# Optimization experiments

Measured on AMD Instinct MI355X. Metric: run time of the kernel, lower is better.

## Reference

```python
import jax, jax.numpy as jnp
import numpy as np

B, T, D, H = 2, 2048, 1024, 16
HD = D // H


def setup_inputs() -> dict:
    key = jax.random.key(0)
    ks = jax.random.split(key, 8)
    s = 1.0 / np.sqrt(D)
    x = jax.random.normal(ks[0], (B, T, D), dtype=jnp.float32)
    # causal additive mask, as in Whisper: -inf-like on strict upper triangle
    mask = jnp.triu(jnp.full((T, T), -1e9, dtype=jnp.float32), k=1)
    Wq = jax.random.normal(ks[1], (D, D), dtype=jnp.float32) * s
    bq = jax.random.normal(ks[2], (D,), dtype=jnp.float32) * 0.02
    Wk = jax.random.normal(ks[3], (D, D), dtype=jnp.float32) * s  # key has no bias
    Wv = jax.random.normal(ks[4], (D, D), dtype=jnp.float32) * s
    bv = jax.random.normal(ks[5], (D,), dtype=jnp.float32) * 0.02
    Wo = jax.random.normal(ks[6], (D, D), dtype=jnp.float32) * s
    bo = jax.random.normal(ks[7], (D,), dtype=jnp.float32) * 0.02
    return {"x": x, "mask": mask, "Wq": Wq, "bq": bq, "Wk": Wk,
            "Wv": Wv, "bv": bv, "Wo": Wo, "bo": bo}


def reference(x, mask, Wq, bq, Wk, Wv, bv, Wo, bo):
    # Linear layers (torch F.linear: x @ W.T + b)
    q = x @ Wq.T + bq                      # [B, T, D]
    k = x @ Wk.T                           # [B, T, D] (no bias)
    v = x @ Wv.T + bv                      # [B, T, D]

    scale = (D // H) ** (-0.25)
    qh = q.reshape(B, T, H, HD) * scale    # [B, T, H, hd]
    kh = k.reshape(B, T, H, HD) * scale
    vh = v.reshape(B, T, H, HD)

    qk = jnp.einsum("bqhd,bkhd->bhqk", qh, kh)        # [B, H, T, T]
    qk = qk + mask[:T, :T]
    w = jax.nn.softmax(qk.astype(jnp.float32), axis=-1).astype(q.dtype)
    wv = jnp.einsum("bhqk,bkhd->bqhd", w, vh).reshape(B, T, D)
    return wv @ Wo.T + bo
```

## Files before the change

kernel.cpp:

```cpp
#include <hip/hip_runtime.h>
#include <hip/hip_bf16.h>

#define B_ 2
#define T_ 2048
#define D_ 1024
#define H_ 16
#define HD_ 64

typedef __attribute__((ext_vector_type(8))) short bf16x8;
typedef __attribute__((ext_vector_type(4))) short bf16x4;
typedef __attribute__((ext_vector_type(4))) float f32x4;
typedef __attribute__((ext_vector_type(4))) unsigned int u32x4;

__device__ __forceinline__ short f2bf(float f) {
  unsigned int u = __builtin_bit_cast(unsigned int, f);
  u += 0x7fffu + ((u >> 16) & 1u);
  return (short)(u >> 16);
}

__device__ __forceinline__ unsigned cvtpk(float lo, float hi) {
  unsigned r;
  asm("v_cvt_pk_bf16_f32 %0, %1, %2" : "=v"(r) : "v"(lo), "v"(hi));
  return r;
}

__device__ __forceinline__ float ex2(float x) {
  float r;
  asm("v_exp_f32 %0, %1" : "=v"(r) : "v"(x));
  return r;
}

__device__ __forceinline__ void gl16(const short* g, short* l) {
  __builtin_amdgcn_global_load_lds(
      (const __attribute__((address_space(1))) void*)g,
      (__attribute__((address_space(3))) void*)l, 16, 0, 0);
}

__global__ void cast_f32_bf16(const float* __restrict__ in, short* __restrict__ out, int n) {
  int i = (blockIdx.x * blockDim.x + threadIdx.x) * 8;
  if (i + 7 >= n) return;
  float4 a = *(const float4*)(in + i);
  float4 b = *(const float4*)(in + i + 4);
  bf16x8 o;
  o[0] = f2bf(a.x); o[1] = f2bf(a.y); o[2] = f2bf(a.z); o[3] = f2bf(a.w);
  o[4] = f2bf(b.x); o[5] = f2bf(b.y); o[6] = f2bf(b.z); o[7] = f2bf(b.w);
  *(bf16x8*)(out + i) = o;
}

__global__ void cast_w4(const float* __restrict__ w0, const float* __restrict__ w1,
                        const float* __restrict__ w2, const float* __restrict__ w3,
                        short* __restrict__ out) {
  int i = (blockIdx.x * blockDim.x + threadIdx.x) * 8;
  int seg = i >> 20;
  const float* src = (seg == 0) ? w0 : (seg == 1) ? w1 : (seg == 2) ? w2 : w3;
  int off = i & 1048575;
  float4 a = *(const float4*)(src + off);
  float4 b = *(const float4*)(src + off + 4);
  bf16x8 o;
  o[0] = f2bf(a.x); o[1] = f2bf(a.y); o[2] = f2bf(a.z); o[3] = f2bf(a.w);
  o[4] = f2bf(b.x); o[5] = f2bf(b.y); o[6] = f2bf(b.z); o[7] = f2bf(b.w);
  *(bf16x8*)(out + i) = o;
}

__launch_bounds__(256, 3)
__global__ void gemm_qkv(const short* __restrict__ A, const short* __restrict__ W,
                         const float* __restrict__ bq, const float* __restrict__ bv,
                         short* __restrict__ Qb, short* __restrict__ Kb,
                         short* __restrict__ Vtb) {
  __shared__ short As[2][64 * 64];
  __shared__ short Bs[2][128 * 64];
  const int bm = blockIdx.x / 24, bn = blockIdx.x % 24;
  const int tid = threadIdx.x, lane = tid & 63, w = tid >> 6;
  const int wr = w >> 1, wc = w & 1;
  const int lrow = lane & 15, lhi = lane >> 4;
  const int srow = lane >> 3, sch = lane & 7;
  const int swz = (lrow & 7) << 3;

  f32x4 acc[2][4] = {};
  auto STAGE = [&](int kt, int buf) {
#pragma unroll
    for (int i = 0; i < 2; ++i) {
      int row = w * 16 + i * 8 + srow;
      gl16(A + (size_t)(bm * 64 + row) * 1024 + kt + ((sch ^ (row & 7)) * 8),
           &As[buf][(w * 16 + i * 8) * 64]);
    }
#pragma unroll
    for (int i = 0; i < 4; ++i) {
      int row = w * 32 + i * 8 + srow;
      gl16(W + (size_t)(bn * 128 + row) * 1024 + kt + ((sch ^ (row & 7)) * 8),
           &Bs[buf][(w * 32 + i * 8) * 64]);
    }
  };

  STAGE(0, 0);
  for (int t = 0; t < 16; ++t) {
    const int buf = t & 1;
    if (t < 15) {
      STAGE((t + 1) * 64, buf ^ 1);
      asm volatile("s_waitcnt vmcnt(6)" ::: "memory");
    } else {
      asm volatile("s_waitcnt vmcnt(0)" ::: "memory");
    }
    __builtin_amdgcn_s_barrier();
    bf16x8 af[2][2], bfr[2][4];
#pragma unroll
    for (int ks = 0; ks < 2; ++ks) {
#pragma unroll
      for (int i = 0; i < 2; ++i)
        af[ks][i] = *(const bf16x8*)(&As[buf][(wr * 32 + i * 16 + lrow) * 64 + ((ks * 32 + lhi * 8) ^ swz)]);
#pragma unroll
      for (int j = 0; j < 4; ++j)
        bfr[ks][j] = *(const bf16x8*)(&Bs[buf][(wc * 64 + j * 16 + lrow) * 64 + ((ks * 32 + lhi * 8) ^ swz)]);
    }
#pragma unroll
    for (int ks = 0; ks < 2; ++ks)
#pragma unroll
      for (int i = 0; i < 2; ++i)
#pragma unroll
        for (int j = 0; j < 4; ++j)
          acc[i][j] = __builtin_amdgcn_mfma_f32_16x16x32_bf16(af[ks][i], bfr[ks][j],
                                                              acc[i][j], 0, 0, 0);
    asm volatile("s_waitcnt lgkmcnt(0)" ::: "memory");
    __builtin_amdgcn_s_barrier();
  }

#pragma unroll
  for (int i = 0; i < 2; ++i)
#pragma unroll
    for (int j = 0; j < 4; ++j) {
      const int m0 = bm * 64 + wr * 32 + i * 16 + lhi * 4;
      const int n = bn * 128 + wc * 64 + j * 16 + lrow;
      const int seg = n >> 10, nloc = n & 1023;
      const int h = nloc >> 6, hd = nloc & 63;
      const int b = m0 >> 11, t0 = m0 & 2047;
      if (seg == 0) {
        float bb = bq[nloc];
#pragma unroll
        for (int r = 0; r < 4; ++r)
          Qb[((size_t)(b * H_ + h) * T_ + t0 + r) * HD_ + hd] =
              f2bf((acc[i][j][r] + bb) * 0.180336880f);
      } else if (seg == 1) {
#pragma unroll
        for (int r = 0; r < 4; ++r)
          Kb[((size_t)(b * H_ + h) * T_ + t0 + r) * HD_ + hd] = f2bf(acc[i][j][r]);
      } else {
        float bb = bv[nloc];
        bf16x4 ov;
#pragma unroll
        for (int r = 0; r < 4; ++r) ov[r] = f2bf(acc[i][j][r] + bb);
        *(bf16x4*)(Vtb + ((size_t)(b * H_ + h) * HD_ + hd) * T_ + t0) = ov;
      }
    }
}

__launch_bounds__(256, 3)
__global__ void gemm_o(const short* __restrict__ A, const short* __restrict__ W,
                       const float* __restrict__ bias, float* __restrict__ out) {
  __shared__ short As[2][64 * 64];
  __shared__ short Bs[2][128 * 64];
  const int bm = blockIdx.x >> 3, bn = blockIdx.x & 7;
  const int tid = threadIdx.x, lane = tid & 63, w = tid >> 6;
  const int wr = w >> 1, wc = w & 1;
  const int lrow = lane & 15, lhi = lane >> 4;
  const int srow = lane >> 3, sch = lane & 7;
  const int swz = (lrow & 7) << 3;

  f32x4 acc[2][4] = {};
  auto STAGE = [&](int kt, int buf) {
#pragma unroll
    for (int i = 0; i < 2; ++i) {
      int row = w * 16 + i * 8 + srow;
      gl16(A + (size_t)(bm * 64 + row) * 1024 + kt + ((sch ^ (row & 7)) * 8),
           &As[buf][(w * 16 + i * 8) * 64]);
    }
#pragma unroll
    for (int i = 0; i < 4; ++i) {
      int row = w * 32 + i * 8 + srow;
      gl16(W + (size_t)(bn * 128 + row) * 1024 + kt + ((sch ^ (row & 7)) * 8),
           &Bs[buf][(w * 32 + i * 8) * 64]);
    }
  };

  STAGE(0, 0);
  for (int t = 0; t < 16; ++t) {
    const int buf = t & 1;
    if (t < 15) {
      STAGE((t + 1) * 64, buf ^ 1);
      asm volatile("s_waitcnt vmcnt(6)" ::: "memory");
    } else {
      asm volatile("s_waitcnt vmcnt(0)" ::: "memory");
    }
    __builtin_amdgcn_s_barrier();
    bf16x8 af[2][2], bfr[2][4];
#pragma unroll
    for (int ks = 0; ks < 2; ++ks) {
#pragma unroll
      for (int i = 0; i < 2; ++i)
        af[ks][i] = *(const bf16x8*)(&As[buf][(wr * 32 + i * 16 + lrow) * 64 + ((ks * 32 + lhi * 8) ^ swz)]);
#pragma unroll
      for (int j = 0; j < 4; ++j)
        bfr[ks][j] = *(const bf16x8*)(&Bs[buf][(wc * 64 + j * 16 + lrow) * 64 + ((ks * 32 + lhi * 8) ^ swz)]);
    }
#pragma unroll
    for (int ks = 0; ks < 2; ++ks)
#pragma unroll
      for (int i = 0; i < 2; ++i)
#pragma unroll
        for (int j = 0; j < 4; ++j)
          acc[i][j] = __builtin_amdgcn_mfma_f32_16x16x32_bf16(af[ks][i], bfr[ks][j],
                                                              acc[i][j], 0, 0, 0);
    asm volatile("s_waitcnt lgkmcnt(0)" ::: "memory");
    __builtin_amdgcn_s_barrier();
  }

#pragma unroll
  for (int i = 0; i < 2; ++i)
#pragma unroll
    for (int j = 0; j < 4; ++j) {
      const int m0 = bm * 64 + wr * 32 + i * 16 + lhi * 4;
      const int n = bn * 128 + wc * 64 + j * 16 + lrow;
      const float bb = bias[n];
#pragma unroll
      for (int r = 0; r < 4; ++r)
        out[(size_t)(m0 + r) * 1024 + n] = acc[i][j][r] + bb;
    }
}

__launch_bounds__(256, 4)
__global__ void attn_kernel(const short* __restrict__ Q, const short* __restrict__ K,
                            const short* __restrict__ Vt, short* __restrict__ Ob) {
  __shared__ short Ks_[2][64 * 64];
  __shared__ short Vs_[2][64 * 64];
  const int tid = threadIdx.x, lane = tid & 63, w = tid >> 6;
  const int lrow = lane & 15, lhi = lane >> 4;
  const int bid = blockIdx.x;
  const int bh = (bid & 7) * 4 + ((bid >> 3) & 3);
  const int x = bid >> 5, g = x & 7, q = x >> 3;
  const int tile = ((q & 1) ? (7 - g) : g) * 4 + q;
  const int b = bh >> 4, h = bh & 15;
  const short* Kbh = K + (size_t)bh * T_ * HD_;
  const short* Vbh = Vt + (size_t)bh * HD_ * T_;

  bf16x8 qf[2];
#pragma unroll
  for (int ks = 0; ks < 2; ++ks)
    qf[ks] = *(const bf16x8*)(Q + ((size_t)bh * T_ + tile * 64 + w * 16 + lrow) * HD_ + ks * 32 + lhi * 8);

  f32x4 oacc[4] = {};
  float lrun = 0.f;
  const int qlocal = w * 16 + lrow;
  const int srow8 = lane >> 3, sch = lane & 7;
  const int swz = (lrow & 7) << 3;

  auto STAGE = [&](int kb, int buf) {
#pragma unroll
    for (int pass = 0; pass < 2; ++pass) {
      int row = pass * 32 + w * 8 + srow8;
      int csrc = (sch ^ (row & 7)) * 8;
      gl16(Kbh + (size_t)(kb * 64 + row) * HD_ + csrc, &Ks_[buf][(pass * 32 + w * 8) * 64]);
      gl16(Vbh + (size_t)row * T_ + kb * 64 + csrc, &Vs_[buf][(pass * 32 + w * 8) * 64]);
    }
  };

  STAGE(0, 0);
  int cur = 0;
  for (int kb = 0; kb <= tile; ++kb) {
    asm volatile("s_waitcnt vmcnt(0) lgkmcnt(0)" ::: "memory");
    __builtin_amdgcn_s_barrier();
    asm volatile("" ::: "memory");
    const short* Kc = Ks_[cur];
    const short* Vc = Vs_[cur];
    bf16x8 kf[4][2];
#pragma unroll
    for (int n = 0; n < 4; ++n)
#pragma unroll
      for (int ks = 0; ks < 2; ++ks)
        kf[n][ks] = *(const bf16x8*)(Kc + (n * 16 + lrow) * 64 + ((ks * 32 + lhi * 8) ^ swz));
    if (kb < tile) STAGE(kb + 1, cur ^ 1);

    f32x4 s[4] = {};
    __builtin_amdgcn_s_setprio(1);
#pragma unroll
    for (int n = 0; n < 4; ++n)
#pragma unroll
      for (int ks = 0; ks < 2; ++ks)
        s[n] = __builtin_amdgcn_mfma_f32_16x16x32_bf16(kf[n][ks], qf[ks], s[n], 0, 0, 0);
    __builtin_amdgcn_s_setprio(0);

    if (kb == tile) {
#pragma unroll
      for (int n = 0; n < 4; ++n)
#pragma unroll
        for (int r = 0; r < 4; ++r)
          if (n * 16 + lhi * 4 + r > qlocal) s[n][r] = -1e9f;
    }

    float p[4][4];
    float ls = 0.f;
#pragma unroll
    for (int n = 0; n < 4; ++n)
#pragma unroll
      for (int r = 0; r < 4; ++r) {
        float e = ex2(s[n][r] - 12.0f);
        p[n][r] = e;
        ls += e;
      }
    lrun += ls;

    u32x4 pw0, pw1;
    pw0[0] = cvtpk(p[0][0], p[0][1]); pw0[1] = cvtpk(p[0][2], p[0][3]);
    pw0[2] = cvtpk(p[1][0], p[1][1]); pw0[3] = cvtpk(p[1][2], p[1][3]);
    pw1[0] = cvtpk(p[2][0], p[2][1]); pw1[1] = cvtpk(p[2][2], p[2][3]);
    pw1[2] = cvtpk(p[3][0], p[3][1]); pw1[3] = cvtpk(p[3][2], p[3][3]);
    bf16x8 pf0 = __builtin_bit_cast(bf16x8, pw0);
    bf16x8 pf1 = __builtin_bit_cast(bf16x8, pw1);

    bf16x8 vf[4][2];
#pragma unroll
    for (int j = 0; j < 4; ++j)
#pragma unroll
      for (int ks = 0; ks < 2; ++ks) {
        bf16x4 lo = *(const bf16x4*)(Vc + (j * 16 + lrow) * 64 + ((ks * 32 + lhi * 4) ^ swz));
        bf16x4 hi = *(const bf16x4*)(Vc + (j * 16 + lrow) * 64 + ((ks * 32 + 16 + lhi * 4) ^ swz));
        bf16x8 v;
        v[0] = lo[0]; v[1] = lo[1]; v[2] = lo[2]; v[3] = lo[3];
        v[4] = hi[0]; v[5] = hi[1]; v[6] = hi[2]; v[7] = hi[3];
        vf[j][ks] = v;
      }
    __builtin_amdgcn_s_setprio(1);
#pragma unroll
    for (int j = 0; j < 4; ++j) {
      oacc[j] = __builtin_amdgcn_mfma_f32_16x16x32_bf16(vf[j][0], pf0, oacc[j], 0, 0, 0);
      oacc[j] = __builtin_amdgcn_mfma_f32_16x16x32_bf16(vf[j][1], pf1, oacc[j], 0, 0, 0);
    }
    __builtin_amdgcn_s_setprio(0);
    cur ^= 1;
  }

  lrun += __shfl_xor(lrun, 16);
  lrun += __shfl_xor(lrun, 32);
  float inv = 1.0f / lrun;
  const int t = tile * 64 + qlocal;
#pragma unroll
  for (int j = 0; j < 4; ++j) {
    bf16x4 ok;
#pragma unroll
    for (int r = 0; r < 4; ++r) ok[r] = f2bf(oacc[j][r] * inv);
    *(bf16x4*)(Ob + (size_t)(b * T_ + t) * D_ + h * 64 + j * 16 + lhi * 4) = ok;
  }
}

extern "C" void kernel_launch(void* const* d_in, const int* in_sizes, int n_in,
                              void* d_out, int out_size, void* d_ws, size_t ws_size,
                              hipStream_t stream) {
  const float* x  = (const float*)d_in[0];
  const float* Wq = (const float*)d_in[2];
  const float* bq = (const float*)d_in[3];
  const float* Wk = (const float*)d_in[4];
  const float* Wv = (const float*)d_in[5];
  const float* bv = (const float*)d_in[6];
  const float* Wo = (const float*)d_in[7];
  const float* bo = (const float*)d_in[8];
  float* out = (float*)d_out;

  const int MT = B_ * T_;
  short* xb  = (short*)d_ws;
  short* wqb = xb  + (size_t)MT * D_;
  short* wkb = wqb + (size_t)D_ * D_;
  short* wvb = wkb + (size_t)D_ * D_;
  short* wob = wvb + (size_t)D_ * D_;
  short* Qb  = wob + (size_t)D_ * D_;
  short* Kb  = Qb  + (size_t)MT * D_;
  short* Vtb = Kb  + (size_t)MT * D_;
  short* Ab  = Vtb + (size_t)MT * D_;

  cast_f32_bf16<<<(MT * D_) / (256 * 8), 256, 0, stream>>>(x, xb, MT * D_);
  cast_w4<<<(4 * D_ * D_) / (256 * 8), 256, 0, stream>>>(Wq, Wk, Wv, Wo, wqb);

  gemm_qkv<<<(MT / 64) * 24, 256, 0, stream>>>(xb, wqb, bq, bv, Qb, Kb, Vtb);

  attn_kernel<<<B_ * H_ * 32, 256, 0, stream>>>(Qb, Kb, Vtb, Ab);

  gemm_o<<<(MT / 64) * 8, 256, 0, stream>>>(Ab, wob, bo, out);
}
```

Baseline: 101.5 us.

## Enlarge GEMM tiles to 128x128, drop double buffering, merge cast kernels

Both projection GEMMs now use 128x128 output tiles with a 4x4 MFMA accumulator per wave instead of 64x128. Each tile loads its operands into a single LDS buffer guarded by __syncthreads, replacing the double-buffered async prefetch. The two f32-to-bf16 cast kernels are merged into one launch covering x and all four weight matrices. Larger tiles raise operand reuse and cut global traffic, but the launch grid halves (256 blocks for gemm_o, 768 for qkv), and removing the prefetch exposes load latency.

```diff
diff --git a/kernel.cpp b/kernel.cpp
--- a/kernel.cpp
+++ b/kernel.cpp
@@ -36,24 +36,20 @@
       (__attribute__((address_space(3))) void*)l, 16, 0, 0);
 }
 
-__global__ void cast_f32_bf16(const float* __restrict__ in, short* __restrict__ out, int n) {
+__global__ void cast_all(const float* __restrict__ x,
+                         const float* __restrict__ w0, const float* __restrict__ w1,
+                         const float* __restrict__ w2, const float* __restrict__ w3,
+                         short* __restrict__ out) {
   int i = (blockIdx.x * blockDim.x + threadIdx.x) * 8;
-  if (i + 7 >= n) return;
-  float4 a = *(const float4*)(in + i);
-  float4 b = *(const float4*)(in + i + 4);
-  bf16x8 o;
-  o[0] = f2bf(a.x); o[1] = f2bf(a.y); o[2] = f2bf(a.z); o[3] = f2bf(a.w);
-  o[4] = f2bf(b.x); o[5] = f2bf(b.y); o[6] = f2bf(b.z); o[7] = f2bf(b.w);
-  *(bf16x8*)(out + i) = o;
-}
-
-__global__ void cast_w4(const float* __restrict__ w0, const float* __restrict__ w1,
-                        const float* __restrict__ w2, const float* __restrict__ w3,
-                        short* __restrict__ out) {
-  int i = (blockIdx.x * blockDim.x + threadIdx.x) * 8;
-  int seg = i >> 20;
-  const float* src = (seg == 0) ? w0 : (seg == 1) ? w1 : (seg == 2) ? w2 : w3;
-  int off = i & 1048575;
+  const float* src;
+  int off;
+  if (i < 4194304) { src = x; off = i; }
+  else {
+    int j = i - 4194304;
+    int seg = j >> 20;
+    src = (seg == 0) ? w0 : (seg == 1) ? w1 : (seg == 2) ? w2 : w3;
+    off = j & 1048575;
+  }
   float4 a = *(const float4*)(src + off);
   float4 b = *(const float4*)(src + off + 4);
   bf16x8 o;
@@ -62,13 +58,13 @@
   *(bf16x8*)(out + i) = o;
 }
 
-__launch_bounds__(256, 3)
+__launch_bounds__(256)
 __global__ void gemm_qkv(const short* __restrict__ A, const short* __restrict__ W,
                          const float* __restrict__ bq, const float* __restrict__ bv,
                          short* __restrict__ Qb, short* __restrict__ Kb,
                          short* __restrict__ Vtb) {
-  __shared__ short As[2][64 * 64];
-  __shared__ short Bs[2][128 * 64];
+  __shared__ short As[128 * 64];
+  __shared__ short Bs[128 * 64];
   const int bm = blockIdx.x / 24, bn = blockIdx.x % 24;
   const int tid = threadIdx.x, lane = tid & 63, w = tid >> 6;
   const int wr = w >> 1, wc = w & 1;
@@ -76,59 +72,43 @@
   const int srow = lane >> 3, sch = lane & 7;
   const int swz = (lrow & 7) << 3;
 
-  f32x4 acc[2][4] = {};
-  auto STAGE = [&](int kt, int buf) {
-#pragma unroll
-    for (int i = 0; i < 2; ++i) {
-      int row = w * 16 + i * 8 + srow;
-      gl16(A + (size_t)(bm * 64 + row) * 1024 + kt + ((sch ^ (row & 7)) * 8),
-           &As[buf][(w * 16 + i * 8) * 64]);
-    }
+  f32x4 acc[4][4] = {};
+
+  for (int t = 0; t < 16; ++t) {
+    const int kt = t * 64;
 #pragma unroll
     for (int i = 0; i < 4; ++i) {
       int row = w * 32 + i * 8 + srow;
+      gl16(A + (size_t)(bm * 128 + row) * 1024 + kt + ((sch ^ (row & 7)) * 8),
+           &As[(w * 32 + i * 8) * 64]);
       gl16(W + (size_t)(bn * 128 + row) * 1024 + kt + ((sch ^ (row & 7)) * 8),
-           &Bs[buf][(w * 32 + i * 8) * 64]);
-    }
-  };
-
-  STAGE(0, 0);
-  for (int t = 0; t < 16; ++t) {
-    const int buf = t & 1;
-    if (t < 15) {
-      STAGE((t + 1) * 64, buf ^ 1);
-      asm volatile("s_waitcnt vmcnt(6)" ::: "memory");
-    } else {
-      asm volatile("s_waitcnt vmcnt(0)" ::: "memory");
-    }
-    __builtin_amdgcn_s_barrier();
-    bf16x8 af[2][2], bfr[2][4];
-#pragma unroll
-    for (int ks = 0; ks < 2; ++ks) {
-#pragma unroll
-      for (int i = 0; i < 2; ++i)
-        af[ks][i] = *(const bf16x8*)(&As[buf][(wr * 32 + i * 16 + lrow) * 64 + ((ks * 32 + lhi * 8) ^ swz)]);
-#pragma unroll
-      for (int j = 0; j < 4; ++j)
-        bfr[ks][j] = *(const bf16x8*)(&Bs[buf][(wc * 64 + j * 16 + lrow) * 64 + ((ks * 32 + lhi * 8) ^ swz)]);
-    }
+           &Bs[(w * 32 + i * 8) * 64]);
+    }
+    __syncthreads();
+    bf16x8 af[2][4], bfr[2][4];
 #pragma unroll
     for (int ks = 0; ks < 2; ++ks)
 #pragma unroll
-      for (int i = 0; i < 2; ++i)
+      for (int i = 0; i < 4; ++i) {
+        af[ks][i]  = *(const bf16x8*)(&As[(wr * 64 + i * 16 + lrow) * 64 + ((ks * 32 + lhi * 8) ^ swz)]);
+        bfr[ks][i] = *(const bf16x8*)(&Bs[(wc * 64 + i * 16 + lrow) * 64 + ((ks * 32 + lhi * 8) ^ swz)]);
+      }
+#pragma unroll
+    for (int ks = 0; ks < 2; ++ks)
+#pragma unroll
+      for (int i = 0; i < 4; ++i)
 #pragma unroll
         for (int j = 0; j < 4; ++j)
           acc[i][j] = __builtin_amdgcn_mfma_f32_16x16x32_bf16(af[ks][i], bfr[ks][j],
                                                               acc[i][j], 0, 0, 0);
-    asm volatile("s_waitcnt lgkmcnt(0)" ::: "memory");
-    __builtin_amdgcn_s_barrier();
-  }
-
-#pragma unroll
-  for (int i = 0; i < 2; ++i)
+    __syncthreads();
+  }
+
+#pragma unroll
+  for (int i = 0; i < 4; ++i)
 #pragma unroll
     for (int j = 0; j < 4; ++j) {
-      const int m0 = bm * 64 + wr * 32 + i * 16 + lhi * 4;
+      const int m0 = bm * 128 + wr * 64 + i * 16 + lhi * 4;
       const int n = bn * 128 + wc * 64 + j * 16 + lrow;
       const int seg = n >> 10, nloc = n & 1023;
       const int h = nloc >> 6, hd = nloc & 63;
@@ -153,11 +133,11 @@
     }
 }
 
-__launch_bounds__(256, 3)
+__launch_bounds__(256)
 __global__ void gemm_o(const short* __restrict__ A, const short* __restrict__ W,
                        const float* __restrict__ bias, float* __restrict__ out) {
-  __shared__ short As[2][64 * 64];
-  __shared__ short Bs[2][128 * 64];
+  __shared__ short As[128 * 64];
+  __shared__ short Bs[128 * 64];
   const int bm = blockIdx.x >> 3, bn = blockIdx.x & 7;
   const int tid = threadIdx.x, lane = tid & 63, w = tid >> 6;
   const int wr = w >> 1, wc = w & 1;
@@ -165,59 +145,43 @@
   const int srow = lane >> 3, sch = lane & 7;
   const int swz = (lrow & 7) << 3;
 
-  f32x4 acc[2][4] = {};
-  auto STAGE = [&](int kt, int buf) {
-#pragma unroll
-    for (int i = 0; i < 2; ++i) {
-      int row = w * 16 + i * 8 + srow;
-      gl16(A + (size_t)(bm * 64 + row) * 1024 + kt + ((sch ^ (row & 7)) * 8),
-           &As[buf][(w * 16 + i * 8) * 64]);
-    }
+  f32x4 acc[4][4] = {};
+
+  for (int t = 0; t < 16; ++t) {
+    const int kt = t * 64;
 #pragma unroll
     for (int i = 0; i < 4; ++i) {
       int row = w * 32 + i * 8 + srow;
+      gl16(A + (size_t)(bm * 128 + row) * 1024 + kt + ((sch ^ (row & 7)) * 8),
+           &As[(w * 32 + i * 8) * 64]);
       gl16(W + (size_t)(bn * 128 + row) * 1024 + kt + ((sch ^ (row & 7)) * 8),
-           &Bs[buf][(w * 32 + i * 8) * 64]);
-    }
-  };
-
-  STAGE(0, 0);
-  for (int t = 0; t < 16; ++t) {
-    const int buf = t & 1;
-    if (t < 15) {
-      STAGE((t + 1) * 64, buf ^ 1);
-      asm volatile("s_waitcnt vmcnt(6)" ::: "memory");
-    } else {
-      asm volatile("s_waitcnt vmcnt(0)" ::: "memory");
-    }
-    __builtin_amdgcn_s_barrier();
-    bf16x8 af[2][2], bfr[2][4];
-#pragma unroll
-    for (int ks = 0; ks < 2; ++ks) {
-#pragma unroll
-      for (int i = 0; i < 2; ++i)
-        af[ks][i] = *(const bf16x8*)(&As[buf][(wr * 32 + i * 16 + lrow) * 64 + ((ks * 32 + lhi * 8) ^ swz)]);
-#pragma unroll
-      for (int j = 0; j < 4; ++j)
-        bfr[ks][j] = *(const bf16x8*)(&Bs[buf][(wc * 64 + j * 16 + lrow) * 64 + ((ks * 32 + lhi * 8) ^ swz)]);
-    }
+           &Bs[(w * 32 + i * 8) * 64]);
+    }
+    __syncthreads();
+    bf16x8 af[2][4], bfr[2][4];
 #pragma unroll
     for (int ks = 0; ks < 2; ++ks)
 #pragma unroll
-      for (int i = 0; i < 2; ++i)
+      for (int i = 0; i < 4; ++i) {
+        af[ks][i]  = *(const bf16x8*)(&As[(wr * 64 + i * 16 + lrow) * 64 + ((ks * 32 + lhi * 8) ^ swz)]);
+        bfr[ks][i] = *(const bf16x8*)(&Bs[(wc * 64 + i * 16 + lrow) * 64 + ((ks * 32 + lhi * 8) ^ swz)]);
+      }
+#pragma unroll
+    for (int ks = 0; ks < 2; ++ks)
+#pragma unroll
+      for (int i = 0; i < 4; ++i)
 #pragma unroll
         for (int j = 0; j < 4; ++j)
           acc[i][j] = __builtin_amdgcn_mfma_f32_16x16x32_bf16(af[ks][i], bfr[ks][j],
                                                               acc[i][j], 0, 0, 0);
-    asm volatile("s_waitcnt lgkmcnt(0)" ::: "memory");
-    __builtin_amdgcn_s_barrier();
-  }
-
-#pragma unroll
-  for (int i = 0; i < 2; ++i)
+    __syncthreads();
+  }
+
+#pragma unroll
+  for (int i = 0; i < 4; ++i)
 #pragma unroll
     for (int j = 0; j < 4; ++j) {
-      const int m0 = bm * 64 + wr * 32 + i * 16 + lhi * 4;
+      const int m0 = bm * 128 + wr * 64 + i * 16 + lhi * 4;
       const int n = bn * 128 + wc * 64 + j * 16 + lrow;
       const float bb = bias[n];
 #pragma unroll
@@ -366,20 +330,17 @@
   const int MT = B_ * T_;
   short* xb  = (short*)d_ws;
   short* wqb = xb  + (size_t)MT * D_;
-  short* wkb = wqb + (size_t)D_ * D_;
-  short* wvb = wkb + (size_t)D_ * D_;
-  short* wob = wvb + (size_t)D_ * D_;
+  short* wob = wqb + (size_t)3 * D_ * D_;
   short* Qb  = wob + (size_t)D_ * D_;
   short* Kb  = Qb  + (size_t)MT * D_;
   short* Vtb = Kb  + (size_t)MT * D_;
   short* Ab  = Vtb + (size_t)MT * D_;
 
-  cast_f32_bf16<<<(MT * D_) / (256 * 8), 256, 0, stream>>>(x, xb, MT * D_);
-  cast_w4<<<(4 * D_ * D_) / (256 * 8), 256, 0, stream>>>(Wq, Wk, Wv, Wo, wqb);
-
-  gemm_qkv<<<(MT / 64) * 24, 256, 0, stream>>>(xb, wqb, bq, bv, Qb, Kb, Vtb);
+  cast_all<<<(8 * 1048576) / (256 * 8), 256, 0, stream>>>(x, Wq, Wk, Wv, Wo, xb);
+
+  gemm_qkv<<<(MT / 128) * 24, 256, 0, stream>>>(xb, wqb, bq, bv, Qb, Kb, Vtb);
 
   attn_kernel<<<B_ * H_ * 32, 256, 0, stream>>>(Qb, Kb, Vtb, Ab);
 
-  gemm_o<<<(MT / 64) * 8, 256, 0, stream>>>(Ab, wob, bo, out);
-}
+  gemm_o<<<(MT / 128) * 8, 256, 0, stream>>>(Ab, wob, bo, out);
+}
```

Measured after the change: 117.6 us. 1.16x slower.

## Merge cast kernels, permute V^T columns for vector LDS reads, drop exp offset

Applied to the files above, without the earlier changes.

Merges the x and weight fp32-to-bf16 casts into one launch. The QKV GEMM now writes V^T with a permuted token order inside each 64-token block, so the attention kernel can read V fragments with a single 16-byte LDS load instead of two 8-byte loads plus shuffles. Those V loads are also moved earlier, next to the K loads and ahead of the next-tile prefetch. The constant -12 shift inside exp2 is removed, which could matter for overflow if scores grow large, but softmax normalization still cancels it.

```diff
diff --git a/kernel.cpp b/kernel.cpp
--- a/kernel.cpp
+++ b/kernel.cpp
@@ -36,24 +36,20 @@
       (__attribute__((address_space(3))) void*)l, 16, 0, 0);
 }
 
-__global__ void cast_f32_bf16(const float* __restrict__ in, short* __restrict__ out, int n) {
+__global__ void cast_all(const float* __restrict__ x,
+                         const float* __restrict__ w0, const float* __restrict__ w1,
+                         const float* __restrict__ w2, const float* __restrict__ w3,
+                         short* __restrict__ out) {
   int i = (blockIdx.x * blockDim.x + threadIdx.x) * 8;
-  if (i + 7 >= n) return;
-  float4 a = *(const float4*)(in + i);
-  float4 b = *(const float4*)(in + i + 4);
-  bf16x8 o;
-  o[0] = f2bf(a.x); o[1] = f2bf(a.y); o[2] = f2bf(a.z); o[3] = f2bf(a.w);
-  o[4] = f2bf(b.x); o[5] = f2bf(b.y); o[6] = f2bf(b.z); o[7] = f2bf(b.w);
-  *(bf16x8*)(out + i) = o;
-}
-
-__global__ void cast_w4(const float* __restrict__ w0, const float* __restrict__ w1,
-                        const float* __restrict__ w2, const float* __restrict__ w3,
-                        short* __restrict__ out) {
-  int i = (blockIdx.x * blockDim.x + threadIdx.x) * 8;
-  int seg = i >> 20;
-  const float* src = (seg == 0) ? w0 : (seg == 1) ? w1 : (seg == 2) ? w2 : w3;
-  int off = i & 1048575;
+  const float* src;
+  int off;
+  if (i < 4194304) { src = x; off = i; }
+  else {
+    int j = i - 4194304;
+    int seg = j >> 20;
+    src = (seg == 0) ? w0 : (seg == 1) ? w1 : (seg == 2) ? w2 : w3;
+    off = j & 1048575;
+  }
   float4 a = *(const float4*)(src + off);
   float4 b = *(const float4*)(src + off + 4);
   bf16x8 o;
@@ -148,7 +144,8 @@
         bf16x4 ov;
 #pragma unroll
         for (int r = 0; r < 4; ++r) ov[r] = f2bf(acc[i][j][r] + bb);
-        *(bf16x4*)(Vtb + ((size_t)(b * H_ + h) * HD_ + hd) * T_ + t0) = ov;
+        const int c = wr * 32 + lhi * 8 + i * 4;
+        *(bf16x4*)(Vtb + ((size_t)(b * H_ + h) * HD_ + hd) * T_ + (t0 & ~63) + c) = ov;
       }
     }
 }
@@ -276,6 +273,12 @@
 #pragma unroll
       for (int ks = 0; ks < 2; ++ks)
         kf[n][ks] = *(const bf16x8*)(Kc + (n * 16 + lrow) * 64 + ((ks * 32 + lhi * 8) ^ swz));
+    bf16x8 vf[4][2];
+#pragma unroll
+    for (int j = 0; j < 4; ++j)
+#pragma unroll
+      for (int ks = 0; ks < 2; ++ks)
+        vf[j][ks] = *(const bf16x8*)(Vc + (j * 16 + lrow) * 64 + ((ks * 32 + lhi * 8) ^ swz));
     if (kb < tile) STAGE(kb + 1, cur ^ 1);
 
     f32x4 s[4] = {};
@@ -301,7 +304,7 @@
     for (int n = 0; n < 4; ++n)
 #pragma unroll
       for (int r = 0; r < 4; ++r) {
-        float e = ex2(s[n][r] - 12.0f);
+        float e = ex2(s[n][r]);
         p[n][r] = e;
         ls += e;
       }
@@ -315,18 +318,6 @@
     bf16x8 pf0 = __builtin_bit_cast(bf16x8, pw0);
     bf16x8 pf1 = __builtin_bit_cast(bf16x8, pw1);
 
-    bf16x8 vf[4][2];
-#pragma unroll
-    for (int j = 0; j < 4; ++j)
-#pragma unroll
-      for (int ks = 0; ks < 2; ++ks) {
-        bf16x4 lo = *(const bf16x4*)(Vc + (j * 16 + lrow) * 64 + ((ks * 32 + lhi * 4) ^ swz));
-        bf16x4 hi = *(const bf16x4*)(Vc + (j * 16 + lrow) * 64 + ((ks * 32 + 16 + lhi * 4) ^ swz));
-        bf16x8 v;
-        v[0] = lo[0]; v[1] = lo[1]; v[2] = lo[2]; v[3] = lo[3];
-        v[4] = hi[0]; v[5] = hi[1]; v[6] = hi[2]; v[7] = hi[3];
-        vf[j][ks] = v;
-      }
     __builtin_amdgcn_s_setprio(1);
 #pragma unroll
     for (int j = 0; j < 4; ++j) {
@@ -366,16 +357,13 @@
   const int MT = B_ * T_;
   short* xb  = (short*)d_ws;
   short* wqb = xb  + (size_t)MT * D_;
-  short* wkb = wqb + (size_t)D_ * D_;
-  short* wvb = wkb + (size_t)D_ * D_;
-  short* wob = wvb + (size_t)D_ * D_;
+  short* wob = wqb + (size_t)3 * D_ * D_;
   short* Qb  = wob + (size_t)D_ * D_;
   short* Kb  = Qb  + (size_t)MT * D_;
   short* Vtb = Kb  + (size_t)MT * D_;
   short* Ab  = Vtb + (size_t)MT * D_;
 
-  cast_f32_bf16<<<(MT * D_) / (256 * 8), 256, 0, stream>>>(x, xb, MT * D_);
-  cast_w4<<<(4 * D_ * D_) / (256 * 8), 256, 0, stream>>>(Wq, Wk, Wv, Wo, wqb);
+  cast_all<<<(8 * 1048576) / (256 * 8), 256, 0, stream>>>(x, Wq, Wk, Wv, Wo, xb);
 
   gemm_qkv<<<(MT / 64) * 24, 256, 0, stream>>>(xb, wqb, bq, bv, Qb, Kb, Vtb);
 
```

Result: faster. 92.62 us (-8.7%).
